# Kernel optimization log

Measured on AMD Instinct MI355X. Metric: run time of the kernel, lower is better.

Reference implementation:

```python
import jax, jax.numpy as jnp
import numpy as np

WS = 7      # window_size
NH = 12     # num_heads
SHIFT = 3   # shift_size

def _rel_pos_index(ws):
    coords = np.stack(np.meshgrid(np.arange(ws), np.arange(ws), indexing='ij')).reshape(2, -1)
    rel = (coords[:, :, None] - coords[:, None, :]).transpose(1, 2, 0)  # [N,N,2]
    rel[..., 0] += ws - 1
    rel[..., 1] += ws - 1
    rel[..., 0] *= 2 * ws - 1
    return jnp.asarray(rel.sum(-1))  # [N,N] int

REL_IDX = _rel_pos_index(WS)

def _ln(x, g, b, eps=1e-5):
    m = x.mean(-1, keepdims=True)
    v = ((x - m) ** 2).mean(-1, keepdims=True)
    return (x - m) / jnp.sqrt(v + eps) * g + b

def setup_inputs() -> dict:
    key = jax.random.key(0)
    ks = jax.random.split(key, 10)
    B, H, W, C = 16, 56, 56, 384
    Dff = 4 * C
    s = 0.02
    return {
        'x': jax.random.normal(ks[0], (B, H * W, C), jnp.float32),
        'norm1_g': jnp.ones((C,), jnp.float32),
        'norm1_b': jnp.zeros((C,), jnp.float32),
        'qkv_w': jax.random.normal(ks[1], (3 * C, C), jnp.float32) * s,
        'qkv_b': jax.random.normal(ks[2], (3 * C,), jnp.float32) * s,
        'proj_w': jax.random.normal(ks[3], (C, C), jnp.float32) * s,
        'proj_b': jax.random.normal(ks[4], (C,), jnp.float32) * s,
        'rpb_table': jax.random.normal(ks[5], ((2 * WS - 1) ** 2, NH), jnp.float32) * s,
        'norm2_g': jnp.ones((C,), jnp.float32),
        'norm2_b': jnp.zeros((C,), jnp.float32),
        'mlp_w1': jax.random.normal(ks[6], (Dff, C), jnp.float32) * s,
        'mlp_b1': jax.random.normal(ks[7], (Dff,), jnp.float32) * s,
        'mlp_w2': jax.random.normal(ks[8], (C, Dff), jnp.float32) * s,
        'mlp_b2': jax.random.normal(ks[9], (C,), jnp.float32) * s,
        'H': H,
        'W': W,
    }

def reference(x, norm1_g, norm1_b, qkv_w, qkv_b, proj_w, proj_b, rpb_table,
              norm2_g, norm2_b, mlp_w1, mlp_b1, mlp_w2, mlp_b2, H, W):
    B, L, C = x.shape
    # --- norm1 + shift + window partition ---
    h = _ln(x, norm1_g, norm1_b).reshape(B, H, W, C)
    h = jnp.roll(h, (-SHIFT, -SHIFT), axis=(1, 2))
    nh, nw = H // WS, W // WS
    xw = h.reshape(B, nh, WS, nw, WS, C).transpose(0, 1, 3, 2, 4, 5).reshape(-1, WS * WS, C)
    # --- window attention with relative position bias ---
    Bw, N, _ = xw.shape
    hd = C // NH
    qkv = (xw @ qkv_w.T + qkv_b).reshape(Bw, N, 3, NH, hd).transpose(2, 0, 3, 1, 4)
    q, k, v = qkv[0] * (hd ** -0.5), qkv[1], qkv[2]  # [Bw,NH,N,hd]
    attn = jnp.einsum('bhnd,bhmd->bhnm', q, k)
    bias = rpb_table[REL_IDX.reshape(-1)].reshape(N, N, NH).transpose(2, 0, 1)  # [NH,N,N]
    attn = jax.nn.softmax(attn + bias[None], axis=-1)
    o = jnp.einsum('bhnm,bhmd->bhnd', attn, v).transpose(0, 2, 1, 3).reshape(Bw, N, C)
    o = o @ proj_w.T + proj_b
    # --- window reverse + unshift + residual ---
    o = o.reshape(B, nh, nw, WS, WS, C).transpose(0, 1, 3, 2, 4, 5).reshape(B, H, W, C)
    o = jnp.roll(o, (SHIFT, SHIFT), axis=(1, 2)).reshape(B, L, C)
    x = x + o
    # --- MLP ---
    h = _ln(x, norm2_g, norm2_b)
    h = jax.nn.gelu(h @ mlp_w1.T + mlp_b1, approximate=False) @ mlp_w2.T + mlp_b2
    return x + h
```

## Files before the change

kernel.cpp:

```cpp
#include <hip/hip_runtime.h>

typedef unsigned short ushort_t;
typedef unsigned int uint32;
typedef __attribute__((ext_vector_type(8))) short short8;
typedef __attribute__((ext_vector_type(4))) float floatx4;

static __device__ __forceinline__ ushort_t f2bf(float f) {
    union { float f; unsigned int u; } c; c.f = f;
    unsigned int u = c.u;
    return (ushort_t)((u + 0x7FFFu + ((u >> 16) & 1u)) >> 16);
}

__global__ __launch_bounds__(256) void cvt_weights(
    const float* __restrict__ w0, const float* __restrict__ w1,
    const float* __restrict__ w2, const float* __restrict__ w3,
    ushort_t* __restrict__ o0, ushort_t* __restrict__ o1,
    ushort_t* __restrict__ o2, ushort_t* __restrict__ o3)
{
    int i = blockIdx.x * 256 + threadIdx.x;
    if (i < 442368) o0[i] = f2bf(w0[i]);
    if (i < 147456) o1[i] = f2bf(w1[i]);
    if (i < 589824) o2[i] = f2bf(w2[i]);
    if (i < 589824) o3[i] = f2bf(w3[i]);
}

__global__ __launch_bounds__(256) void build_bias(
    const float* __restrict__ rpb, float* __restrict__ biasM)
{
    int idx = blockIdx.x * 256 + threadIdx.x;
    int h = idx >> 12, q = (idx >> 6) & 63, j = idx & 63;
    float v = 0.f;
    if (q < 49 && j < 49) {
        int pi = q / 7, pj = q - pi * 7;
        int qi = j / 7, qj = j - qi * 7;
        v = rpb[((pi - qi + 6) * 13 + (pj - qj + 6)) * 12 + h];
    }
    biasM[idx] = v;
}

template<bool WPART>
__global__ __launch_bounds__(256) void ln_kernel(
    const float* __restrict__ x, const float* __restrict__ g,
    const float* __restrict__ b, ushort_t* __restrict__ out)
{
    int wave = threadIdx.x >> 6, lane = threadIdx.x & 63;
    int tkn = blockIdx.x * 4 + wave;
    const float* src;
    if (WPART) {
        int w = tkn / 49, n = tkn - w * 49;
        int bb = w >> 6, wrem = w & 63;
        int wi = wrem >> 3, wj = wrem & 7;
        int pi = n / 7, pj = n - pi * 7;
        int si = wi * 7 + pi + 3; if (si >= 56) si -= 56;
        int sj = wj * 7 + pj + 3; if (sj >= 56) sj -= 56;
        src = x + ((size_t)bb * 3136 + si * 56 + sj) * 384;
    } else {
        src = x + (size_t)tkn * 384;
    }
    float v[6];
    float s = 0.f, sq = 0.f;
#pragma unroll
    for (int it = 0; it < 3; ++it) {
        float2 t = *(const float2*)(src + it * 128 + lane * 2);
        v[it * 2] = t.x; v[it * 2 + 1] = t.y;
        s += t.x + t.y; sq += t.x * t.x + t.y * t.y;
    }
#pragma unroll
    for (int off = 32; off; off >>= 1) {
        s += __shfl_xor(s, off, 64);
        sq += __shfl_xor(sq, off, 64);
    }
    float mean = s * (1.f / 384.f);
    float rstd = rsqrtf(sq * (1.f / 384.f) - mean * mean + 1e-5f);
    ushort_t* dst = out + (size_t)tkn * 384;
#pragma unroll
    for (int it = 0; it < 3; ++it) {
        int c = it * 128 + lane * 2;
        float2 gg = *(const float2*)(g + c);
        float2 bb2 = *(const float2*)(b + c);
        float y0 = (v[it * 2] - mean) * rstd * gg.x + bb2.x;
        float y1 = (v[it * 2 + 1] - mean) * rstd * gg.y + bb2.y;
        uint32 pack = ((uint32)f2bf(y0)) | (((uint32)f2bf(y1)) << 16);
        *(uint32*)(dst + c) = pack;
    }
}

template<int EPI>
__global__ __launch_bounds__(256) void gemm_bt(
    const ushort_t* __restrict__ A, const ushort_t* __restrict__ Bw,
    const float* __restrict__ bias, void* __restrict__ out,
    const float* __restrict__ resid, int M, int N, int K)
{
    __shared__ __align__(16) ushort_t As[64][72];
    __shared__ __align__(16) ushort_t Bs[64][72];
    int tid = threadIdx.x;
    int bm = blockIdx.y, bn = blockIdx.x;
    int wv = tid >> 6, lane = tid & 63;
    int wrow = wv >> 1, wcol = wv & 1;
    int quad = lane >> 4, l15 = lane & 15;
    int r0 = tid >> 3, s0 = tid & 7;

    floatx4 acc[2][2];
#pragma unroll
    for (int mi = 0; mi < 2; ++mi)
#pragma unroll
        for (int ni = 0; ni < 2; ++ni)
            acc[mi][ni] = (floatx4){0.f, 0.f, 0.f, 0.f};

    int nK = K >> 6;
    for (int kt = 0; kt < nK; ++kt) {
        int k0 = kt << 6;
        uint4 a0 = *(const uint4*)(A + (size_t)(bm * 64 + r0) * K + k0 + s0 * 8);
        uint4 a1 = *(const uint4*)(A + (size_t)(bm * 64 + r0 + 32) * K + k0 + s0 * 8);
        uint4 b0 = *(const uint4*)(Bw + (size_t)(bn * 64 + r0) * K + k0 + s0 * 8);
        uint4 b1 = *(const uint4*)(Bw + (size_t)(bn * 64 + r0 + 32) * K + k0 + s0 * 8);
        *(uint4*)&As[r0][s0 * 8] = a0;
        *(uint4*)&As[r0 + 32][s0 * 8] = a1;
        *(uint4*)&Bs[r0][s0 * 8] = b0;
        *(uint4*)&Bs[r0 + 32][s0 * 8] = b1;
        __syncthreads();
#pragma unroll
        for (int kk = 0; kk < 64; kk += 32) {
            short8 af[2], bfr[2];
            af[0] = *(const short8*)&As[wrow * 32 + l15][kk + quad * 8];
            af[1] = *(const short8*)&As[wrow * 32 + 16 + l15][kk + quad * 8];
            bfr[0] = *(const short8*)&Bs[wcol * 32 + l15][kk + quad * 8];
            bfr[1] = *(const short8*)&Bs[wcol * 32 + 16 + l15][kk + quad * 8];
#pragma unroll
            for (int mi = 0; mi < 2; ++mi)
#pragma unroll
                for (int ni = 0; ni < 2; ++ni)
                    acc[mi][ni] = __builtin_amdgcn_mfma_f32_16x16x32_bf16(
                        af[mi], bfr[ni], acc[mi][ni], 0, 0, 0);
        }
        __syncthreads();
    }

#pragma unroll
    for (int mi = 0; mi < 2; ++mi) {
#pragma unroll
        for (int ni = 0; ni < 2; ++ni) {
            int gn = bn * 64 + wcol * 32 + ni * 16 + l15;
            float bv = bias[gn];
#pragma unroll
            for (int r = 0; r < 4; ++r) {
                int gm = bm * 64 + wrow * 32 + mi * 16 + quad * 4 + r;
                float v = acc[mi][ni][r] + bv;
                if (EPI == 0) {
                    if (gn < 384) v *= 0.17677669529663689f;
                    ((ushort_t*)out)[(size_t)gm * N + gn] = f2bf(v);
                } else if (EPI == 1) {
                    v = 0.5f * v * (1.f + erff(v * 0.70710678118654752f));
                    ((ushort_t*)out)[(size_t)gm * N + gn] = f2bf(v);
                } else if (EPI == 2) {
                    int wdx = gm / 49, n = gm - wdx * 49;
                    int b = wdx >> 6, wrem = wdx & 63;
                    int wi = wrem >> 3, wj = wrem & 7;
                    int pi = n / 7, pj = n - pi * 7;
                    int i = wi * 7 + pi + 3; if (i >= 56) i -= 56;
                    int j = wj * 7 + pj + 3; if (j >= 56) j -= 56;
                    size_t dst = ((size_t)b * 3136 + i * 56 + j) * 384 + gn;
                    ((float*)out)[dst] = resid[dst] + v;
                } else {
                    size_t dst = (size_t)gm * 384 + gn;
                    ((float*)out)[dst] = resid[dst] + v;
                }
            }
        }
    }
}

__global__ __launch_bounds__(256) void attn_kernel(
    const ushort_t* __restrict__ qkv,
    const float* __restrict__ biasM,
    ushort_t* __restrict__ O)
{
    __shared__ __align__(16) ushort_t Pl[4][64][72];
    __shared__ __align__(16) ushort_t Vt[4][32][72];
    int wave = threadIdx.x >> 6;
    int lane = threadIdx.x & 63;
    int id = blockIdx.x * 4 + wave;
    int w = id / 12, h = id % 12;
    int quad = lane >> 4, l15 = lane & 15;
    ushort_t (*P)[72] = Pl[wave];
    ushort_t (*V)[72] = Vt[wave];

    for (int i = lane; i < 32 * 16; i += 64) {
        int d = i >> 4, j = 48 + (i & 15);
        V[d][j] = 0;
    }
    for (int idx = lane; idx < 49 * 4; idx += 64) {
        int j = idx >> 2, seg = idx & 3;
        const ushort_t* src = qkv + (size_t)(w * 49 + j) * 1152 + 768 + h * 32 + seg * 8;
        uint4 u = *(const uint4*)src;
        const ushort_t* tmp = (const ushort_t*)&u;
#pragma unroll
        for (int t = 0; t < 8; ++t) V[seg * 8 + t][j] = tmp[t];
    }

    short8 aQ[4], bK[4];
#pragma unroll
    for (int t = 0; t < 4; ++t) {
        int row = t * 16 + l15; if (row > 48) row = 48;
        aQ[t] = *(const short8*)(qkv + (size_t)(w * 49 + row) * 1152 + h * 32 + quad * 8);
        bK[t] = *(const short8*)(qkv + (size_t)(w * 49 + row) * 1152 + 384 + h * 32 + quad * 8);
    }
    floatx4 S[4][4];
    floatx4 z4 = (floatx4){0.f, 0.f, 0.f, 0.f};
#pragma unroll
    for (int mt = 0; mt < 4; ++mt)
#pragma unroll
        for (int nt = 0; nt < 4; ++nt)
            S[mt][nt] = __builtin_amdgcn_mfma_f32_16x16x32_bf16(aQ[mt], bK[nt], z4, 0, 0, 0);

    const float* bh = biasM + h * 4096;
#pragma unroll
    for (int mt = 0; mt < 4; ++mt) {
#pragma unroll
        for (int r = 0; r < 4; ++r) {
            int q = mt * 16 + quad * 4 + r;
            float mx = -1e30f;
#pragma unroll
            for (int nt = 0; nt < 4; ++nt) {
                int j = nt * 16 + l15;
                float sv = S[mt][nt][r] + bh[q * 64 + j];
                if (j >= 49) sv = -1e30f;
                S[mt][nt][r] = sv;
                mx = fmaxf(mx, sv);
            }
#pragma unroll
            for (int off = 1; off < 16; off <<= 1) mx = fmaxf(mx, __shfl_xor(mx, off, 64));
            float sum = 0.f;
#pragma unroll
            for (int nt = 0; nt < 4; ++nt) {
                int j = nt * 16 + l15;
                float p = __expf(S[mt][nt][r] - mx);
                if (j >= 49) p = 0.f;
                S[mt][nt][r] = p;
                sum += p;
            }
#pragma unroll
            for (int off = 1; off < 16; off <<= 1) sum += __shfl_xor(sum, off, 64);
            float inv = 1.f / sum;
#pragma unroll
            for (int nt = 0; nt < 4; ++nt) {
                int j = nt * 16 + l15;
                P[q][j] = f2bf(S[mt][nt][r] * inv);
            }
        }
    }
    __syncthreads();

    short8 aV[2][2];
#pragma unroll
    for (int mt = 0; mt < 2; ++mt)
#pragma unroll
        for (int kt = 0; kt < 2; ++kt)
            aV[mt][kt] = *(const short8*)&V[mt * 16 + l15][kt * 32 + quad * 8];
    floatx4 Oc[2][4];
#pragma unroll
    for (int mt = 0; mt < 2; ++mt)
#pragma unroll
        for (int nt = 0; nt < 4; ++nt)
            Oc[mt][nt] = z4;
#pragma unroll
    for (int nt = 0; nt < 4; ++nt) {
#pragma unroll
        for (int kt = 0; kt < 2; ++kt) {
            short8 bP = *(const short8*)&P[nt * 16 + l15][kt * 32 + quad * 8];
#pragma unroll
            for (int mt = 0; mt < 2; ++mt)
                Oc[mt][nt] = __builtin_amdgcn_mfma_f32_16x16x32_bf16(
                    aV[mt][kt], bP, Oc[mt][nt], 0, 0, 0);
        }
    }
#pragma unroll
    for (int nt = 0; nt < 4; ++nt) {
        int query = nt * 16 + l15;
        if (query < 49) {
#pragma unroll
            for (int mt = 0; mt < 2; ++mt) {
                ushort4 pk;
                pk.x = f2bf(Oc[mt][nt][0]);
                pk.y = f2bf(Oc[mt][nt][1]);
                pk.z = f2bf(Oc[mt][nt][2]);
                pk.w = f2bf(Oc[mt][nt][3]);
                *(ushort4*)(O + (size_t)(w * 49 + query) * 384 + h * 32 + mt * 16 + quad * 4) = pk;
            }
        }
    }
}

extern "C" void kernel_launch(void* const* d_in, const int* in_sizes, int n_in,
                              void* d_out, int out_size, void* d_ws, size_t ws_size,
                              hipStream_t stream) {
    const float* x      = (const float*)d_in[0];
    const float* n1g    = (const float*)d_in[1];
    const float* n1b    = (const float*)d_in[2];
    const float* qkv_w  = (const float*)d_in[3];
    const float* qkv_b  = (const float*)d_in[4];
    const float* proj_w = (const float*)d_in[5];
    const float* proj_b = (const float*)d_in[6];
    const float* rpb    = (const float*)d_in[7];
    const float* n2g    = (const float*)d_in[8];
    const float* n2b    = (const float*)d_in[9];
    const float* w1     = (const float*)d_in[10];
    const float* b1     = (const float*)d_in[11];
    const float* w2     = (const float*)d_in[12];
    const float* b2     = (const float*)d_in[13];
    float* out = (float*)d_out;
    char* ws = (char*)d_ws;

    ushort_t* qkvbuf = (ushort_t*)ws;
    ushort_t* bufA   = (ushort_t*)(ws + 115605504);
    ushort_t* wq     = (ushort_t*)(ws + 154140672);
    ushort_t* wp     = wq + 442368;
    ushort_t* wm1    = wp + 147456;
    ushort_t* wm2    = wm1 + 589824;
    float* biasM     = (float*)(ws + 154140672 + 3538944);

    cvt_weights<<<2304, 256, 0, stream>>>(qkv_w, proj_w, w1, w2, wq, wp, wm1, wm2);
    build_bias<<<192, 256, 0, stream>>>(rpb, biasM);

    ln_kernel<true><<<12544, 256, 0, stream>>>(x, n1g, n1b, bufA);
    gemm_bt<0><<<dim3(18, 784), 256, 0, stream>>>(bufA, wq, qkv_b, qkvbuf, nullptr, 50176, 1152, 384);
    attn_kernel<<<3072, 256, 0, stream>>>(qkvbuf, biasM, bufA);
    gemm_bt<2><<<dim3(6, 784), 256, 0, stream>>>(bufA, wp, proj_b, out, x, 50176, 384, 384);
    ln_kernel<false><<<12544, 256, 0, stream>>>(out, n2g, n2b, bufA);
    for (int half = 0; half < 2; ++half) {
        size_t mo = (size_t)half * 25088;
        gemm_bt<1><<<dim3(24, 392), 256, 0, stream>>>(bufA + mo * 384, wm1, b1, qkvbuf, nullptr, 25088, 1536, 384);
        gemm_bt<3><<<dim3(6, 392), 256, 0, stream>>>(qkvbuf, wm2, b2, out + mo * 384, out + mo * 384, 25088, 384, 1536);
    }
}
```

Measured before the change: 677.9 us.

## Enlarge GEMM tiles to 128x128 and load via direct global-to-LDS

The bf16 GEMM tile grows from 64x64 to 128x128, with each wave computing a 64x64 sub-tile of 4x4 MFMA accumulators for more operand reuse per LDS read. Global loads now go straight into LDS through global_load_lds, skipping the register round trip, and the padded LDS rows are dropped. Grid sizes are halved in each dimension to match. In exchange, the unpadded layout may cause LDS bank conflicts, register pressure rises, and the number of blocks is smaller.

```diff
diff --git a/kernel.cpp b/kernel.cpp
--- a/kernel.cpp
+++ b/kernel.cpp
@@ -9,6 +9,12 @@
     union { float f; unsigned int u; } c; c.f = f;
     unsigned int u = c.u;
     return (ushort_t)((u + 0x7FFFu + ((u >> 16) & 1u)) >> 16);
+}
+
+static __device__ __forceinline__ void gload_lds16(const ushort_t* g, ushort_t* l) {
+    __builtin_amdgcn_global_load_lds(
+        (const __attribute__((address_space(1))) unsigned int*)g,
+        (__attribute__((address_space(3))) unsigned int*)l, 16, 0, 0);
 }
 
 __global__ __launch_bounds__(256) void cvt_weights(
@@ -91,45 +97,48 @@
     const float* __restrict__ bias, void* __restrict__ out,
     const float* __restrict__ resid, int M, int N, int K)
 {
-    __shared__ __align__(16) ushort_t As[64][72];
-    __shared__ __align__(16) ushort_t Bs[64][72];
+    __shared__ __align__(16) ushort_t As[128 * 64];
+    __shared__ __align__(16) ushort_t Bs[128 * 64];
     int tid = threadIdx.x;
     int bm = blockIdx.y, bn = blockIdx.x;
     int wv = tid >> 6, lane = tid & 63;
-    int wrow = wv >> 1, wcol = wv & 1;
+    int wr = wv >> 1, wc = wv & 1;
     int quad = lane >> 4, l15 = lane & 15;
-    int r0 = tid >> 3, s0 = tid & 7;
-
-    floatx4 acc[2][2];
-#pragma unroll
-    for (int mi = 0; mi < 2; ++mi)
-#pragma unroll
-        for (int ni = 0; ni < 2; ++ni)
+    int lrow = lane >> 3, lcol = lane & 7;
+
+    floatx4 acc[4][4];
+#pragma unroll
+    for (int mi = 0; mi < 4; ++mi)
+#pragma unroll
+        for (int ni = 0; ni < 4; ++ni)
             acc[mi][ni] = (floatx4){0.f, 0.f, 0.f, 0.f};
+
+    const ushort_t* Ag = A + (size_t)(bm * 128 + wv * 32 + lrow) * K + lcol * 8;
+    const ushort_t* Bg = Bw + (size_t)(bn * 128 + wv * 32 + lrow) * K + lcol * 8;
 
     int nK = K >> 6;
     for (int kt = 0; kt < nK; ++kt) {
         int k0 = kt << 6;
-        uint4 a0 = *(const uint4*)(A + (size_t)(bm * 64 + r0) * K + k0 + s0 * 8);
-        uint4 a1 = *(const uint4*)(A + (size_t)(bm * 64 + r0 + 32) * K + k0 + s0 * 8);
-        uint4 b0 = *(const uint4*)(Bw + (size_t)(bn * 64 + r0) * K + k0 + s0 * 8);
-        uint4 b1 = *(const uint4*)(Bw + (size_t)(bn * 64 + r0 + 32) * K + k0 + s0 * 8);
-        *(uint4*)&As[r0][s0 * 8] = a0;
-        *(uint4*)&As[r0 + 32][s0 * 8] = a1;
-        *(uint4*)&Bs[r0][s0 * 8] = b0;
-        *(uint4*)&Bs[r0 + 32][s0 * 8] = b1;
+#pragma unroll
+        for (int t = 0; t < 4; ++t)
+            gload_lds16(Ag + (size_t)(t * 8) * K + k0, &As[(wv * 4 + t) * 512]);
+#pragma unroll
+        for (int t = 0; t < 4; ++t)
+            gload_lds16(Bg + (size_t)(t * 8) * K + k0, &Bs[(wv * 4 + t) * 512]);
         __syncthreads();
 #pragma unroll
         for (int kk = 0; kk < 64; kk += 32) {
-            short8 af[2], bfr[2];
-            af[0] = *(const short8*)&As[wrow * 32 + l15][kk + quad * 8];
-            af[1] = *(const short8*)&As[wrow * 32 + 16 + l15][kk + quad * 8];
-            bfr[0] = *(const short8*)&Bs[wcol * 32 + l15][kk + quad * 8];
-            bfr[1] = *(const short8*)&Bs[wcol * 32 + 16 + l15][kk + quad * 8];
-#pragma unroll
-            for (int mi = 0; mi < 2; ++mi)
-#pragma unroll
-                for (int ni = 0; ni < 2; ++ni)
+            short8 af[4], bfr[4];
+#pragma unroll
+            for (int mi = 0; mi < 4; ++mi)
+                af[mi] = *(const short8*)&As[(wr * 64 + mi * 16 + l15) * 64 + kk + quad * 8];
+#pragma unroll
+            for (int ni = 0; ni < 4; ++ni)
+                bfr[ni] = *(const short8*)&Bs[(wc * 64 + ni * 16 + l15) * 64 + kk + quad * 8];
+#pragma unroll
+            for (int mi = 0; mi < 4; ++mi)
+#pragma unroll
+                for (int ni = 0; ni < 4; ++ni)
                     acc[mi][ni] = __builtin_amdgcn_mfma_f32_16x16x32_bf16(
                         af[mi], bfr[ni], acc[mi][ni], 0, 0, 0);
         }
@@ -137,14 +146,14 @@
     }
 
 #pragma unroll
-    for (int mi = 0; mi < 2; ++mi) {
-#pragma unroll
-        for (int ni = 0; ni < 2; ++ni) {
-            int gn = bn * 64 + wcol * 32 + ni * 16 + l15;
+    for (int mi = 0; mi < 4; ++mi) {
+#pragma unroll
+        for (int ni = 0; ni < 4; ++ni) {
+            int gn = bn * 128 + wc * 64 + ni * 16 + l15;
             float bv = bias[gn];
 #pragma unroll
             for (int r = 0; r < 4; ++r) {
-                int gm = bm * 64 + wrow * 32 + mi * 16 + quad * 4 + r;
+                int gm = bm * 128 + wr * 64 + mi * 16 + quad * 4 + r;
                 float v = acc[mi][ni][r] + bv;
                 if (EPI == 0) {
                     if (gn < 384) v *= 0.17677669529663689f;
@@ -323,13 +332,13 @@
     build_bias<<<192, 256, 0, stream>>>(rpb, biasM);
 
     ln_kernel<true><<<12544, 256, 0, stream>>>(x, n1g, n1b, bufA);
-    gemm_bt<0><<<dim3(18, 784), 256, 0, stream>>>(bufA, wq, qkv_b, qkvbuf, nullptr, 50176, 1152, 384);
+    gemm_bt<0><<<dim3(9, 392), 256, 0, stream>>>(bufA, wq, qkv_b, qkvbuf, nullptr, 50176, 1152, 384);
     attn_kernel<<<3072, 256, 0, stream>>>(qkvbuf, biasM, bufA);
-    gemm_bt<2><<<dim3(6, 784), 256, 0, stream>>>(bufA, wp, proj_b, out, x, 50176, 384, 384);
+    gemm_bt<2><<<dim3(3, 392), 256, 0, stream>>>(bufA, wp, proj_b, out, x, 50176, 384, 384);
     ln_kernel<false><<<12544, 256, 0, stream>>>(out, n2g, n2b, bufA);
     for (int half = 0; half < 2; ++half) {
         size_t mo = (size_t)half * 25088;
-        gemm_bt<1><<<dim3(24, 392), 256, 0, stream>>>(bufA + mo * 384, wm1, b1, qkvbuf, nullptr, 25088, 1536, 384);
-        gemm_bt<3><<<dim3(6, 392), 256, 0, stream>>>(qkvbuf, wm2, b2, out + mo * 384, out + mo * 384, 25088, 384, 1536);
-    }
-}
+        gemm_bt<1><<<dim3(12, 196), 256, 0, stream>>>(bufA + mo * 384, wm1, b1, qkvbuf, nullptr, 25088, 1536, 384);
+        gemm_bt<3><<<dim3(3, 196), 256, 0, stream>>>(qkvbuf, wm2, b2, out + mo * 384, out + mo * 384, 25088, 384, 1536);
+    }
+}
```

Result: slower. 708.2 us (+4.5%).
